# Optimization experiments

Measured on AMD Instinct MI355X. Metric: run time of the kernel, lower is better.

The kernel has to match this reference:

```python
import jax, jax.numpy as jnp
import numpy as np

NDIM = (256, 256, 256)
NMIN = (-1.0, -1.0, -1.0)
NMAX = (1.0, 1.0, 1.0)
NDELTA = tuple((NMAX[i] - NMIN[i]) / (NDIM[i] - 1.0) for i in range(3))
MIN_DEG, MAX_DEG = 0, 10
ANNEALED_ALPHA = 1.0
EPS = 1e-12


def compute_grad(grid):
    # central differences on the voxel grid with edge padding -> [N, 3]
    g = grid.reshape(NDIM[0], NDIM[1], NDIM[2])
    p = jnp.pad(g, ((1, 1), (1, 1), (1, 1)), mode='edge')
    dx = (p[2:, 1:-1, 1:-1] - p[:-2, 1:-1, 1:-1]) / (2.0 * NDELTA[0])
    dy = (p[1:-1, 2:, 1:-1] - p[1:-1, :-2, 1:-1]) / (2.0 * NDELTA[1])
    dz = (p[1:-1, 1:-1, 2:] - p[1:-1, 1:-1, :-2]) / (2.0 * NDELTA[2])
    return jnp.stack([dx, dy, dz], axis=-1).reshape(-1, 3)


def trilinear3(data, pts):
    # data: [N, 4] flattened voxel features, pts: [B, 3] -> [B, 4]
    x = (pts[..., 0] - NMIN[0]) / NDELTA[0]
    y = (pts[..., 1] - NMIN[1]) / NDELTA[1]
    z = (pts[..., 2] - NMIN[2]) / NDELTA[2]
    x0f = jnp.floor(x); y0f = jnp.floor(y); z0f = jnp.floor(z)
    xd = (x - x0f)[..., None]
    yd = (y - y0f)[..., None]
    zd = (z - z0f)[..., None]
    x0 = jnp.clip(x0f.astype(jnp.int32), 0, NDIM[0] - 1)
    x1 = jnp.clip(x0f.astype(jnp.int32) + 1, 0, NDIM[0] - 1)
    y0 = jnp.clip(y0f.astype(jnp.int32), 0, NDIM[1] - 1)
    y1 = jnp.clip(y0f.astype(jnp.int32) + 1, 0, NDIM[1] - 1)
    z0 = jnp.clip(z0f.astype(jnp.int32), 0, NDIM[2] - 1)
    z1 = jnp.clip(z0f.astype(jnp.int32) + 1, 0, NDIM[2] - 1)
    sYZ, sZ = NDIM[1] * NDIM[2], NDIM[2]
    gat = lambda i, j, k: data[sYZ * i + sZ * j + k]
    c00 = gat(x0, y0, z0) * (1 - xd) + gat(x1, y0, z0) * xd
    c01 = gat(x0, y0, z1) * (1 - xd) + gat(x1, y0, z1) * xd
    c10 = gat(x0, y1, z0) * (1 - xd) + gat(x1, y1, z0) * xd
    c11 = gat(x0, y1, z1) * (1 - xd) + gat(x1, y1, z1) * xd
    c0 = c00 * (1 - yd) + c10 * yd
    c1 = c01 * (1 - yd) + c11 * yd
    return c0 * (1 - zd) + c1 * zd


def annealed_pos_enc(x, alpha):
    # nerfies-style windowed positional encoding with identity concat
    bands = jnp.arange(MIN_DEG, MAX_DEG, dtype=x.dtype)  # [D]
    scales = 2.0 ** bands
    xb = x[..., None, :] * scales[:, None]               # [..., D, 3]
    four = jnp.sin(jnp.stack([xb, xb + 0.5 * jnp.pi], axis=-2))  # [..., D, 2, 3]
    w = jnp.clip(alpha - bands, 0.0, 1.0)
    w = 0.5 * (1.0 - jnp.cos(jnp.pi * w))                # cosine easing window
    four = four * w[:, None, None]
    four = four.reshape(x.shape[:-1] + (-1,))            # [..., D*6]
    return jnp.concatenate([x, four], axis=-1)           # [..., 3 + D*6]


def mlp(feats, w0, b0, w1, b1, w2, b2, w3, b3, wo, bo):
    # net_depth=4, skip_layer=2 -> concat inputs after layer index 2
    h = jax.nn.relu(feats @ w0 + b0)
    h = jax.nn.relu(h @ w1 + b1)
    h = jax.nn.relu(h @ w2 + b2)
    h = jnp.concatenate([h, feats], axis=-1)
    h = jax.nn.relu(h @ w3 + b3)
    return h @ wo + bo


def safe_l2_norm(v):
    return jnp.sqrt(jnp.sum(v * v, axis=-1, keepdims=True) + EPS)


def setup_inputs() -> dict:
    key = jax.random.key(0)
    ks = jax.random.split(key, 8)
    B = 1048576
    N = NDIM[0] * NDIM[1] * NDIM[2]
    x = jax.random.uniform(ks[0], (B, 3), jnp.float32, -1.0, 1.0)
    grid = jax.random.normal(ks[1], (N, 1), jnp.float32)
    glorot = lambda k, fi, fo: jax.random.normal(k, (fi, fo), jnp.float32) * jnp.sqrt(2.0 / (fi + fo))
    return {
        'x': x, 'grid': grid,
        'w0': glorot(ks[2], 63, 128), 'b0': jnp.zeros((128,), jnp.float32),
        'w1': glorot(ks[3], 128, 128), 'b1': jnp.zeros((128,), jnp.float32),
        'w2': glorot(ks[4], 128, 128), 'b2': jnp.zeros((128,), jnp.float32),
        'w3': glorot(ks[5], 191, 128), 'b3': jnp.zeros((128,), jnp.float32),
        'wo': jax.random.normal(ks[6], (128, 3), jnp.float32) * 1e-5,  # output_init normal(1e-5)
        'bo': jnp.zeros((3,), jnp.float32),
    }


def reference(x, grid, w0, b0, w1, b1, w2, b2, w3, b3, wo, bo):
    data = jnp.concatenate([grid, compute_grad(grid)], axis=-1)  # [N, 4]
    ret = trilinear3(data, x)                                    # [B, 4]
    feats = annealed_pos_enc(x[:, None], ANNEALED_ALPHA * MAX_DEG)  # [B, 1, 63]
    raw = mlp(feats, w0, b0, w1, b1, w2, b2, w3, b3, wo, bo)[:, 0]  # [B, 3]
    # residual + direct output: rotate gradient vector by axis-angle raw
    theta = safe_l2_norm(raw)
    e = raw / theta
    cond = ret[..., 1:]
    a = safe_l2_norm(cond)
    v = cond / a
    rot = a * (jnp.cos(theta) * v + jnp.sin(theta) * jnp.cross(e, v)
               + (1.0 - jnp.cos(theta)) * jnp.sum(e * v, axis=-1, keepdims=True) * e)
    return (ret[..., :1], ret[..., 1:], rot)
```

## Files before the change

kernel.cpp:

```cpp
#include <hip/hip_runtime.h>


typedef __attribute__((ext_vector_type(4))) float f4;
typedef long long llg;
typedef __attribute__((ext_vector_type(2))) long long llg2;

#define MFMA8 __builtin_amdgcn_mfma_f32_16x16x32_fp8_fp8
#define SCHED_FENCE() __builtin_amdgcn_sched_barrier(0)

__device__ __forceinline__ float bf2f(unsigned int u) {
    union { float f; unsigned int i; } v; v.i = u << 16; return v.f;
}
__device__ __forceinline__ unsigned int pkbf(float a, float b) {
    unsigned int r;
    asm("v_cvt_pk_bf16_f32 %0, %1, %2" : "=v"(r) : "v"(a), "v"(b));
    return r;
}
__device__ __forceinline__ float vfract(float a) {
    float d; asm("v_fract_f32 %0, %1" : "=v"(d) : "v"(a)); return d;
}
__device__ __forceinline__ float vsin(float a) {
    float d; asm("v_sin_f32 %0, %1" : "=v"(d) : "v"(a)); return d;
}
__device__ __forceinline__ float gv(const float* __restrict__ g, int i, int j, int k) {
    return g[(i * 256 + j) * 256 + k];
}
__device__ __forceinline__ int featmap(int kp) {
    if (kp < 3) return kp;
    if (kp == 3) return -1;
    const int m = kp - 4, b = m / 6, r = m - 6 * b, d = r >> 1, c = r & 1;
    return 3 + 6 * b + 3 * c + d;
}
__device__ __forceinline__ int hidperm(int k) {
    const int kt = k >> 5, q = (k >> 3) & 3, j = k & 7;
    return 32 * kt + ((j >> 2) << 4) + (q << 2) + (j & 3);
}
__device__ __forceinline__ llg mkllg(unsigned int lo, unsigned int hi) {
    return (llg)(((unsigned long long)lo) | (((unsigned long long)hi) << 32));
}
__device__ __forceinline__ unsigned int pack8(f4 acc) {
    int d = __builtin_amdgcn_cvt_pk_fp8_f32(fmaxf(acc[0], 0.f), fmaxf(acc[1], 0.f), 0, false);
    d     = __builtin_amdgcn_cvt_pk_fp8_f32(fmaxf(acc[2], 0.f), fmaxf(acc[3], 0.f), d, true);
    return (unsigned int)d;
}

#define WS_TOTAL 67584
#define SWZ_BLOCKS 264
#define DG_BLOCKS 8192
#define DG_OFF_SH 131072
#define WS_NEED (262144ull + 16777216ull * 8ull)
#define WO_SCALE 8192.0f
#define WO_INV   (1.0f / 8192.0f)
#define INV2PI 0.15915494309189535f

__global__ __launch_bounds__(256) void prep(
    const float* __restrict__ g,
    const float* __restrict__ w0, const float* __restrict__ w1,
    const float* __restrict__ w2, const float* __restrict__ w3,
    const float* __restrict__ wo,
    unsigned char* __restrict__ ws8, unsigned short* __restrict__ dg,
    int do_dgrid)
{
    const int bid = blockIdx.x;
    if (bid < SWZ_BLOCKS) {
        int idx = bid * 256 + threadIdx.x;
        const float* src; int base, KTP, Kact, Nact, ld;
        if (idx < 8192)       { src = w0; base = 0;     KTP = 1; Kact = 64;  Nact = 128; ld = 128; }
        else if (idx < 24576) { src = w1; base = 8192;  KTP = 2; Kact = 128; Nact = 128; ld = 128; }
        else if (idx < 40960) { src = w2; base = 24576; KTP = 2; Kact = 128; Nact = 128; ld = 128; }
        else if (idx < 65536) { src = w3; base = 40960; KTP = 3; Kact = 192; Nact = 128; ld = 128; }
        else                  { src = wo; base = 65536; KTP = 2; Kact = 128; Nact = 3;   ld = 3;   }
        int local = idx - base;
        int j    = local & 7;
        int half = (local >> 3) & 1;
        int lane = (local >> 4) & 63;
        int c    = local >> 10;
        int ktp  = c % KTP, nt = c / KTP;
        int kt   = ktp * 2 + half;
        int k = kt * 32 + ((lane >> 4) << 3) + j;
        int n = nt * 16 + (lane & 15);
        float v = 0.0f;
        if (k < Kact && n < Nact) {
            int ko;
            if (base == 0) {
                ko = featmap(k);
            } else if (base == 40960) {
                if (k >= 128) {
                    int f = featmap(k - 128);
                    ko = (f < 0) ? -1 : 128 + f;
                } else {
                    ko = hidperm(k);
                }
            } else {
                ko = hidperm(k);
            }
            if (ko >= 0) v = src[ko * ld + n];
            if (base == 65536) v *= WO_SCALE;
        }
        int p = __builtin_amdgcn_cvt_pk_fp8_f32(v, v, 0, false);
        ws8[idx] = (unsigned char)(p & 0xff);
    } else if (do_dgrid) {
        const int t  = (bid - SWZ_BLOCKS) * 256 + threadIdx.x;
        const int k0 = (t & 31) << 3;
        const int j  = (t >> 5) & 255;
        const int i  = t >> 13;
        const float* row = g + (i * 256 + j) * 256;
        const float* rxp = g + (min(i + 1, 255) * 256 + j) * 256;
        const float* rxm = g + (max(i - 1, 0)   * 256 + j) * 256;
        const float* ryp = g + (i * 256 + min(j + 1, 255)) * 256;
        const float* rym = g + (i * 256 + max(j - 1, 0))   * 256;
        float se[8], sxp[8], sxm[8], syp[8], sym[8];
        {
            f4 a = *(const f4*)(row + k0), b = *(const f4*)(row + k0 + 4);
            #pragma unroll
            for (int q = 0; q < 4; ++q) { se[q] = a[q]; se[q + 4] = b[q]; }
            a = *(const f4*)(rxp + k0); b = *(const f4*)(rxp + k0 + 4);
            #pragma unroll
            for (int q = 0; q < 4; ++q) { sxp[q] = a[q]; sxp[q + 4] = b[q]; }
            a = *(const f4*)(rxm + k0); b = *(const f4*)(rxm + k0 + 4);
            #pragma unroll
            for (int q = 0; q < 4; ++q) { sxm[q] = a[q]; sxm[q + 4] = b[q]; }
            a = *(const f4*)(ryp + k0); b = *(const f4*)(ryp + k0 + 4);
            #pragma unroll
            for (int q = 0; q < 4; ++q) { syp[q] = a[q]; syp[q + 4] = b[q]; }
            a = *(const f4*)(rym + k0); b = *(const f4*)(rym + k0 + 4);
            #pragma unroll
            for (int q = 0; q < 4; ++q) { sym[q] = a[q]; sym[q + 4] = b[q]; }
        }
        float zv[10];
        zv[0] = row[max(k0 - 1, 0)];
        #pragma unroll
        for (int q = 0; q < 8; ++q) zv[q + 1] = se[q];
        zv[9] = row[min(k0 + 8, 255)];
        unsigned int o[16];
        #pragma unroll
        for (int q = 0; q < 8; ++q) {
            o[q * 2 + 0] = pkbf(se[q], (sxp[q] - sxm[q]) * 63.75f);
            o[q * 2 + 1] = pkbf((syp[q] - sym[q]) * 63.75f, (zv[q + 2] - zv[q]) * 63.75f);
        }
        unsigned short* dst = dg + (size_t)(((i * 256 + j) * 256 + k0)) * 4;
        #pragma unroll
        for (int q = 0; q < 4; ++q)
            *(uint4*)(dst + q * 8) = *(const uint4*)(&o[q * 4]);
    }
}

#define FSTRIDE_B 88
#define WV_BYTES (32 * FSTRIDE_B)

#define HIDDEN_LAYER(WSL, BIASP, SRCP, DSTP)                                    \
    do {                                                                        \
        _Pragma("unroll")                                                       \
        for (int utp = 0; utp < 4; ++utp) {                                     \
            const int utA = 2 * utp, utB = 2 * utp + 1;                         \
            llg2 wa0 = *(const llg2*)((WSL) + ((utA * 2 + 0) * 64 + lane) * 16);\
            llg2 wa1 = *(const llg2*)((WSL) + ((utA * 2 + 1) * 64 + lane) * 16);\
            llg2 wb0 = *(const llg2*)((WSL) + ((utB * 2 + 0) * 64 + lane) * 16);\
            llg2 wb1 = *(const llg2*)((WSL) + ((utB * 2 + 1) * 64 + lane) * 16);\
            const f4 biasA = *(const f4*)((BIASP) + utA * 16 + quad * 4);       \
            const f4 biasB = *(const f4*)((BIASP) + utB * 16 + quad * 4);       \
            _Pragma("unroll")                                                   \
            for (int pt = 0; pt < 2; ++pt) {                                    \
                f4 a0 = biasA, a1 = biasB;                                      \
                a0 = MFMA8(wa0[0], SRCP[pt][0], a0, 0, 0, 0);                   \
                a0 = MFMA8(wa0[1], SRCP[pt][1], a0, 0, 0, 0);                   \
                a0 = MFMA8(wa1[0], SRCP[pt][2], a0, 0, 0, 0);                   \
                a0 = MFMA8(wa1[1], SRCP[pt][3], a0, 0, 0, 0);                   \
                a1 = MFMA8(wb0[0], SRCP[pt][0], a1, 0, 0, 0);                   \
                a1 = MFMA8(wb0[1], SRCP[pt][1], a1, 0, 0, 0);                   \
                a1 = MFMA8(wb1[0], SRCP[pt][2], a1, 0, 0, 0);                   \
                a1 = MFMA8(wb1[1], SRCP[pt][3], a1, 0, 0, 0);                   \
                DSTP[pt][utp] = mkllg(pack8(a0), pack8(a1));                    \
            }                                                                   \
            SCHED_FENCE();                                                      \
        }                                                                       \
    } while (0)

template<bool FAST>
__global__ __launch_bounds__(256, 5) void voxmlp(
    const float* __restrict__ x, const float* __restrict__ grid,
    const unsigned char* __restrict__ ws8, const unsigned short* __restrict__ dg,
    const float* __restrict__ b0, const float* __restrict__ b1,
    const float* __restrict__ b2, const float* __restrict__ b3,
    const float* __restrict__ bo,
    float* __restrict__ out, int B)
{
    __shared__ unsigned char smem[WV_BYTES * 4];

    const int lane = threadIdx.x & 63;
    const int wave = threadIdx.x >> 6;
    const int quad = lane >> 4;
    const int lm   = lane & 15;
    unsigned char* fbuf = smem + wave * WV_BYTES;

    const int pbase = blockIdx.x * 128 + wave * 32;

    const int p2   = lane & 31;
    const int role = lane >> 5;
    const int pid  = pbase + p2;

    const float px = x[pid * 3 + 0];
    const float py = x[pid * 3 + 1];
    const float pz = x[pid * 3 + 2];

    if (role == 0) {
        const float fx = (px + 1.0f) * 127.5f;
        const float fy = (py + 1.0f) * 127.5f;
        const float fz = (pz + 1.0f) * 127.5f;
        const float fx0 = floorf(fx), fy0 = floorf(fy), fz0 = floorf(fz);
        const float xd = fx - fx0, yd = fy - fy0, zd = fz - fz0;
        const int ix0 = min(max((int)fx0, 0), 255);
        const int iy0 = min(max((int)fy0, 0), 255);
        const int iz0 = min(max((int)fz0, 0), 255);
        const int ix1 = min(ix0 + 1, 255);
        const int iy1 = min(iy0 + 1, 255);
        const int iz1 = min(iz0 + 1, 255);

        float ret0 = 0.f, c1 = 0.f, c2 = 0.f, c3 = 0.f;
        if (FAST) {
            const unsigned char* dgb = (const unsigned char*)dg;
            const unsigned int vbase = (unsigned int)((ix0 * 65536 + iy0 * 256 + iz0) << 3);
            const unsigned int ox = (unsigned int)((ix1 - ix0) << 19);
            const unsigned int oy = (unsigned int)((iy1 - iy0) << 11);
            const unsigned int oz = (unsigned int)((iz1 - iz0) << 3);
            #pragma unroll
            for (int c = 0; c < 8; ++c) {
                const float wgt = ((c & 4) ? xd : 1.0f - xd) *
                                  ((c & 2) ? yd : 1.0f - yd) *
                                  ((c & 1) ? zd : 1.0f - zd);
                const unsigned int off = vbase + ((c & 4) ? ox : 0u)
                                               + ((c & 2) ? oy : 0u)
                                               + ((c & 1) ? oz : 0u);
                const uint2 w = *(const uint2*)(dgb + off);
                ret0 = fmaf(wgt, bf2f(w.x & 0xffffu), ret0);
                c1   = fmaf(wgt, bf2f(w.x >> 16),     c1);
                c2   = fmaf(wgt, bf2f(w.y & 0xffffu), c2);
                c3   = fmaf(wgt, bf2f(w.y >> 16),     c3);
            }
        } else {
            #pragma unroll
            for (int c = 0; c < 8; ++c) {
                const int i = (c & 4) ? ix1 : ix0;
                const int j = (c & 2) ? iy1 : iy0;
                const int k = (c & 1) ? iz1 : iz0;
                const float wgt = ((c & 4) ? xd : 1.0f - xd) *
                                  ((c & 2) ? yd : 1.0f - yd) *
                                  ((c & 1) ? zd : 1.0f - zd);
                const float v  = gv(grid, i, j, k);
                const float gx = (gv(grid, min(i + 1, 255), j, k) - gv(grid, max(i - 1, 0), j, k)) * 63.75f;
                const float gy = (gv(grid, i, min(j + 1, 255), k) - gv(grid, i, max(j - 1, 0), k)) * 63.75f;
                const float gz = (gv(grid, i, j, min(k + 1, 255)) - gv(grid, i, j, max(k - 1, 0))) * 63.75f;
                ret0 = fmaf(wgt, v,  ret0);
                c1   = fmaf(wgt, gx, c1);
                c2   = fmaf(wgt, gy, c2);
                c3   = fmaf(wgt, gz, c3);
            }
        }
        out[pid] = ret0;
        out[B + pid * 3 + 0] = c1;
        out[B + pid * 3 + 1] = c2;
        out[B + pid * 3 + 2] = c3;
        float* cst = (float*)(fbuf + p2 * FSTRIDE_B + 64);
        cst[0] = c1; cst[1] = c2; cst[2] = c3;
    } else {
        const float r0 = px * INV2PI, r1 = py * INV2PI, r2 = pz * INV2PI;
        unsigned char* fb = fbuf + p2 * FSTRIDE_B;
        auto slotv = [&](int n) -> float {
            if (n == 0) return px;
            if (n == 1) return py;
            if (n == 2) return pz;
            if (n == 3) return 0.0f;
            const int m = n - 4, b = m / 6, t = m % 6, ax = t >> 1, ph = t & 1;
            const float rr = (ax == 0) ? r0 : (ax == 1) ? r1 : r2;
            const float arg = rr * (float)(1 << b) + (ph ? 0.25f : 0.0f);
            return vsin(vfract(arg));
        };
        #pragma unroll
        for (int w = 0; w < 8; ++w) {
            int lo = __builtin_amdgcn_cvt_pk_fp8_f32(slotv(8 * w + 0), slotv(8 * w + 1), 0, false);
            lo     = __builtin_amdgcn_cvt_pk_fp8_f32(slotv(8 * w + 2), slotv(8 * w + 3), lo, true);
            int hi = __builtin_amdgcn_cvt_pk_fp8_f32(slotv(8 * w + 4), slotv(8 * w + 5), 0, false);
            hi     = __builtin_amdgcn_cvt_pk_fp8_f32(slotv(8 * w + 6), slotv(8 * w + 7), hi, true);
            uint2 pk; pk.x = (unsigned int)lo; pk.y = (unsigned int)hi;
            *(uint2*)(fb + w * 8) = pk;
        }
    }
    __builtin_amdgcn_s_barrier();

    const int frow0 = lm * FSTRIDE_B + quad * 8;

    llg actA[2][4];
    llg actB[2][4];
    llg ffp[2][2];

    #pragma unroll
    for (int pt = 0; pt < 2; ++pt)
        #pragma unroll
        for (int kt = 0; kt < 2; ++kt)
            ffp[pt][kt] = *(const llg*)(fbuf + pt * 16 * FSTRIDE_B + frow0 + kt * 32);

    #pragma unroll
    for (int utp = 0; utp < 4; ++utp) {
        const int utA = 2 * utp, utB = 2 * utp + 1;
        llg2 wA = *(const llg2*)(ws8 + (utA * 64 + lane) * 16);
        llg2 wB = *(const llg2*)(ws8 + (utB * 64 + lane) * 16);
        const f4 biasA = *(const f4*)(b0 + utA * 16 + quad * 4);
        const f4 biasB = *(const f4*)(b0 + utB * 16 + quad * 4);
        #pragma unroll
        for (int pt = 0; pt < 2; ++pt) {
            f4 a0 = biasA, a1 = biasB;
            a0 = MFMA8(wA[0], ffp[pt][0], a0, 0, 0, 0);
            a0 = MFMA8(wA[1], ffp[pt][1], a0, 0, 0, 0);
            a1 = MFMA8(wB[0], ffp[pt][0], a1, 0, 0, 0);
            a1 = MFMA8(wB[1], ffp[pt][1], a1, 0, 0, 0);
            actA[pt][utp] = mkllg(pack8(a0), pack8(a1));
        }
        SCHED_FENCE();
    }

    HIDDEN_LAYER(ws8 + 8192,  b1, actA, actB);
    HIDDEN_LAYER(ws8 + 24576, b2, actB, actA);

    #pragma unroll
    for (int utp = 0; utp < 4; ++utp) {
        const int utA = 2 * utp, utB = 2 * utp + 1;
        llg2 ha0 = *(const llg2*)(ws8 + 40960 + ((utA * 3 + 0) * 64 + lane) * 16);
        llg2 ha1 = *(const llg2*)(ws8 + 40960 + ((utA * 3 + 1) * 64 + lane) * 16);
        llg2 ha2 = *(const llg2*)(ws8 + 40960 + ((utA * 3 + 2) * 64 + lane) * 16);
        llg2 hb0 = *(const llg2*)(ws8 + 40960 + ((utB * 3 + 0) * 64 + lane) * 16);
        llg2 hb1 = *(const llg2*)(ws8 + 40960 + ((utB * 3 + 1) * 64 + lane) * 16);
        llg2 hb2 = *(const llg2*)(ws8 + 40960 + ((utB * 3 + 2) * 64 + lane) * 16);
        const f4 biasA = *(const f4*)(b3 + utA * 16 + quad * 4);
        const f4 biasB = *(const f4*)(b3 + utB * 16 + quad * 4);
        #pragma unroll
        for (int pt = 0; pt < 2; ++pt) {
            f4 a0 = biasA, a1 = biasB;
            a0 = MFMA8(ha0[0], actA[pt][0], a0, 0, 0, 0);
            a0 = MFMA8(ha0[1], actA[pt][1], a0, 0, 0, 0);
            a0 = MFMA8(ha1[0], actA[pt][2], a0, 0, 0, 0);
            a0 = MFMA8(ha1[1], actA[pt][3], a0, 0, 0, 0);
            a0 = MFMA8(ha2[0], ffp[pt][0],  a0, 0, 0, 0);
            a0 = MFMA8(ha2[1], ffp[pt][1],  a0, 0, 0, 0);
            a1 = MFMA8(hb0[0], actA[pt][0], a1, 0, 0, 0);
            a1 = MFMA8(hb0[1], actA[pt][1], a1, 0, 0, 0);
            a1 = MFMA8(hb1[0], actA[pt][2], a1, 0, 0, 0);
            a1 = MFMA8(hb1[1], actA[pt][3], a1, 0, 0, 0);
            a1 = MFMA8(hb2[0], ffp[pt][0],  a1, 0, 0, 0);
            a1 = MFMA8(hb2[1], ffp[pt][1],  a1, 0, 0, 0);
            actB[pt][utp] = mkllg(pack8(a0), pack8(a1));
        }
        SCHED_FENCE();
    }

    const llg2 o0 = *(const llg2*)(ws8 + 65536 + (lane * 16));
    const llg2 o1 = *(const llg2*)(ws8 + 65536 + ((64 + lane) * 16));

    const float bo0 = bo[0], bo1 = bo[1], bo2 = bo[2];
    #pragma unroll
    for (int pt = 0; pt < 2; ++pt) {
        f4 acc = {0.f, 0.f, 0.f, 0.f};
        acc = MFMA8(o0[0], actB[pt][0], acc, 0, 0, 0);
        acc = MFMA8(o0[1], actB[pt][1], acc, 0, 0, 0);
        acc = MFMA8(o1[0], actB[pt][2], acc, 0, 0, 0);
        acc = MFMA8(o1[1], actB[pt][3], acc, 0, 0, 0);

        const int pp = pt * 16 + lm;
        const float* cst = (const float*)(fbuf + pp * FSTRIDE_B + 64);
        const float g1 = cst[0], g2 = cst[1], g3 = cst[2];
        const float r0 = acc[0] * WO_INV + bo0;
        const float r1 = acc[1] * WO_INV + bo1;
        const float r2 = acc[2] * WO_INV + bo2;
        const float theta = sqrtf(fmaf(r0, r0, fmaf(r1, r1, r2 * r2)) + 1e-12f);
        const float it = __builtin_amdgcn_rcpf(theta);
        const float e0 = r0 * it, e1 = r1 * it, e2 = r2 * it;
        const float a = sqrtf(fmaf(g1, g1, fmaf(g2, g2, g3 * g3)) + 1e-12f);
        const float ia = __builtin_amdgcn_rcpf(a);
        const float v0 = g1 * ia, v1 = g2 * ia, v2 = g3 * ia;
        const float rv = theta * INV2PI;
        const float st = vsin(vfract(rv));
        const float ct = vsin(vfract(rv + 0.25f));
        const float cx = e1 * v2 - e2 * v1;
        const float cy = e2 * v0 - e0 * v2;
        const float cz = e0 * v1 - e1 * v0;
        const float om = (1.0f - ct) * (e0 * v0 + e1 * v1 + e2 * v2);
        if (quad == 0) {
            const int pid2 = pbase + pp;
            out[4 * B + pid2 * 3 + 0] = a * (ct * v0 + st * cx + om * e0);
            out[4 * B + pid2 * 3 + 1] = a * (ct * v1 + st * cy + om * e1);
            out[4 * B + pid2 * 3 + 2] = a * (ct * v2 + st * cz + om * e2);
        }
    }
}

extern "C" void kernel_launch(void* const* d_in, const int* in_sizes, int n_in,
                              void* d_out, int out_size, void* d_ws, size_t ws_size,
                              hipStream_t stream)
{
    const float* x    = (const float*)d_in[0];
    const float* grid = (const float*)d_in[1];
    const float* w0   = (const float*)d_in[2];
    const float* b0   = (const float*)d_in[3];
    const float* w1   = (const float*)d_in[4];
    const float* b1   = (const float*)d_in[5];
    const float* w2   = (const float*)d_in[6];
    const float* b2   = (const float*)d_in[7];
    const float* w3   = (const float*)d_in[8];
    const float* b3   = (const float*)d_in[9];
    const float* wo   = (const float*)d_in[10];
    const float* bo   = (const float*)d_in[11];
    float* out = (float*)d_out;
    unsigned char* ws8 = (unsigned char*)d_ws;
    unsigned short* dg = (unsigned short*)d_ws + DG_OFF_SH;

    const int B = in_sizes[0] / 3;
    const int fast = (ws_size >= WS_NEED) ? 1 : 0;
    const int nprep = fast ? (SWZ_BLOCKS + DG_BLOCKS) : SWZ_BLOCKS;
    prep<<<nprep, 256, 0, stream>>>(grid, w0, w1, w2, w3, wo, ws8, dg, fast);
    if (fast)
        voxmlp<true><<<B / 128, 256, 0, stream>>>(x, grid, ws8, dg, b0, b1, b2, b3, bo, out, B);
    else
        voxmlp<false><<<B / 128, 256, 0, stream>>>(x, grid, ws8, dg, b0, b1, b2, b3, bo, out, B);
}
```

Measured before the change: 322.1 us.

## Process two 32-point batches per wave to amortize weight loads and gathers

Each wave now handles 64 points (two 32-point sub-batches) instead of 32, so the grid shrinks by half. Trilinear gathers for both batches are issued together (role 0 lanes) and positional encoding for both is computed by role 1 lanes. The MLP body then runs twice back to back, reusing the same weight loads from cache. LDS per block doubles, and running the MLP twice serially may raise register pressure and reduce occupancy; B must now be divisible by 256.

```diff
diff --git a/kernel.cpp b/kernel.cpp
--- a/kernel.cpp
+++ b/kernel.cpp
@@ -4,6 +4,7 @@
 typedef __attribute__((ext_vector_type(4))) float f4;
 typedef long long llg;
 typedef __attribute__((ext_vector_type(2))) long long llg2;
+typedef unsigned long long u64;
 
 #define MFMA8 __builtin_amdgcn_mfma_f32_16x16x32_fp8_fp8
 #define SCHED_FENCE() __builtin_amdgcn_sched_barrier(0)
@@ -147,6 +148,68 @@
 
 #define FSTRIDE_B 88
 #define WV_BYTES (32 * FSTRIDE_B)
+#define WV2 (2 * WV_BYTES)
+
+#define TRI_SETUP(S, PX, PY, PZ)                                               \
+    const float fx##S = ((PX) + 1.0f) * 127.5f;                                \
+    const float fy##S = ((PY) + 1.0f) * 127.5f;                                \
+    const float fz##S = ((PZ) + 1.0f) * 127.5f;                                \
+    const float fx0##S = floorf(fx##S), fy0##S = floorf(fy##S), fz0##S = floorf(fz##S); \
+    const float xd##S = fx##S - fx0##S, yd##S = fy##S - fy0##S, zd##S = fz##S - fz0##S; \
+    const int ix0##S = min(max((int)fx0##S, 0), 255);                          \
+    const int iy0##S = min(max((int)fy0##S, 0), 255);                          \
+    const int iz0##S = min(max((int)fz0##S, 0), 255);                          \
+    const int ix1##S = min(ix0##S + 1, 255);                                   \
+    const int iy1##S = min(iy0##S + 1, 255);                                   \
+    const int iz1##S = min(iz0##S + 1, 255);
+
+#define POSENC(PX, PY, PZ, FB)                                                 \
+    do {                                                                       \
+        const float r0_ = (PX) * INV2PI, r1_ = (PY) * INV2PI, r2_ = (PZ) * INV2PI; \
+        unsigned char* fb_ = (FB);                                             \
+        auto slotv_ = [&](int n) -> float {                                    \
+            if (n == 0) return (PX);                                           \
+            if (n == 1) return (PY);                                           \
+            if (n == 2) return (PZ);                                           \
+            if (n == 3) return 0.0f;                                           \
+            const int m_ = n - 4, b_ = m_ / 6, t_ = m_ % 6, ax_ = t_ >> 1, ph_ = t_ & 1; \
+            const float rr_ = (ax_ == 0) ? r0_ : (ax_ == 1) ? r1_ : r2_;       \
+            const float arg_ = rr_ * (float)(1 << b_) + (ph_ ? 0.25f : 0.0f);  \
+            return vsin(vfract(arg_));                                         \
+        };                                                                     \
+        _Pragma("unroll")                                                      \
+        for (int w_ = 0; w_ < 8; ++w_) {                                       \
+            int lo_ = __builtin_amdgcn_cvt_pk_fp8_f32(slotv_(8 * w_ + 0), slotv_(8 * w_ + 1), 0, false); \
+            lo_     = __builtin_amdgcn_cvt_pk_fp8_f32(slotv_(8 * w_ + 2), slotv_(8 * w_ + 3), lo_, true); \
+            int hi_ = __builtin_amdgcn_cvt_pk_fp8_f32(slotv_(8 * w_ + 4), slotv_(8 * w_ + 5), 0, false); \
+            hi_     = __builtin_amdgcn_cvt_pk_fp8_f32(slotv_(8 * w_ + 6), slotv_(8 * w_ + 7), hi_, true); \
+            uint2 pk_; pk_.x = (unsigned int)lo_; pk_.y = (unsigned int)hi_;   \
+            *(uint2*)(fb_ + w_ * 8) = pk_;                                     \
+        }                                                                      \
+    } while (0)
+
+#define CONSUME(S, GL, PIDX, FB)                                               \
+    do {                                                                       \
+        float ret0_ = 0.f, c1_ = 0.f, c2_ = 0.f, c3_ = 0.f;                    \
+        _Pragma("unroll")                                                      \
+        for (int c_ = 0; c_ < 8; ++c_) {                                       \
+            const float wgt_ = ((c_ & 4) ? xd##S : 1.0f - xd##S) *             \
+                               ((c_ & 2) ? yd##S : 1.0f - yd##S) *             \
+                               ((c_ & 1) ? zd##S : 1.0f - zd##S);              \
+            const unsigned int wx_ = (unsigned int)(GL)[c_];                   \
+            const unsigned int wy_ = (unsigned int)((GL)[c_] >> 32);           \
+            ret0_ = fmaf(wgt_, bf2f(wx_ & 0xffffu), ret0_);                    \
+            c1_   = fmaf(wgt_, bf2f(wx_ >> 16),     c1_);                      \
+            c2_   = fmaf(wgt_, bf2f(wy_ & 0xffffu), c2_);                      \
+            c3_   = fmaf(wgt_, bf2f(wy_ >> 16),     c3_);                      \
+        }                                                                      \
+        out[(PIDX)] = ret0_;                                                   \
+        out[B + (PIDX) * 3 + 0] = c1_;                                         \
+        out[B + (PIDX) * 3 + 1] = c2_;                                         \
+        out[B + (PIDX) * 3 + 2] = c3_;                                         \
+        float* cst_ = (float*)((FB) + p2 * FSTRIDE_B + 64);                    \
+        cst_[0] = c1_; cst_[1] = c2_; cst_[2] = c3_;                           \
+    } while (0)
 
 #define HIDDEN_LAYER(WSL, BIASP, SRCP, DSTP)                                    \
     do {                                                                        \
@@ -176,6 +239,105 @@
         }                                                                       \
     } while (0)
 
+#define MLP_BODY(FBUF, PB)                                                      \
+    do {                                                                        \
+        const int frow0 = lm * FSTRIDE_B + quad * 8;                            \
+        llg actA[2][4];                                                         \
+        llg actB[2][4];                                                         \
+        llg ffp[2][2];                                                          \
+        _Pragma("unroll")                                                       \
+        for (int pt = 0; pt < 2; ++pt)                                          \
+            _Pragma("unroll")                                                   \
+            for (int kt = 0; kt < 2; ++kt)                                      \
+                ffp[pt][kt] = *(const llg*)((FBUF) + pt * 16 * FSTRIDE_B + frow0 + kt * 32); \
+        _Pragma("unroll")                                                       \
+        for (int utp = 0; utp < 4; ++utp) {                                     \
+            const int utA = 2 * utp, utB = 2 * utp + 1;                         \
+            llg2 wA = *(const llg2*)(ws8 + (utA * 64 + lane) * 16);             \
+            llg2 wB = *(const llg2*)(ws8 + (utB * 64 + lane) * 16);             \
+            const f4 biasA = *(const f4*)(b0 + utA * 16 + quad * 4);            \
+            const f4 biasB = *(const f4*)(b0 + utB * 16 + quad * 4);            \
+            _Pragma("unroll")                                                   \
+            for (int pt = 0; pt < 2; ++pt) {                                    \
+                f4 a0 = biasA, a1 = biasB;                                      \
+                a0 = MFMA8(wA[0], ffp[pt][0], a0, 0, 0, 0);                     \
+                a0 = MFMA8(wA[1], ffp[pt][1], a0, 0, 0, 0);                     \
+                a1 = MFMA8(wB[0], ffp[pt][0], a1, 0, 0, 0);                     \
+                a1 = MFMA8(wB[1], ffp[pt][1], a1, 0, 0, 0);                     \
+                actA[pt][utp] = mkllg(pack8(a0), pack8(a1));                    \
+            }                                                                   \
+            SCHED_FENCE();                                                      \
+        }                                                                       \
+        HIDDEN_LAYER(ws8 + 8192,  b1, actA, actB);                              \
+        HIDDEN_LAYER(ws8 + 24576, b2, actB, actA);                              \
+        _Pragma("unroll")                                                       \
+        for (int utp = 0; utp < 4; ++utp) {                                     \
+            const int utA = 2 * utp, utB = 2 * utp + 1;                         \
+            llg2 ha0 = *(const llg2*)(ws8 + 40960 + ((utA * 3 + 0) * 64 + lane) * 16); \
+            llg2 ha1 = *(const llg2*)(ws8 + 40960 + ((utA * 3 + 1) * 64 + lane) * 16); \
+            llg2 ha2 = *(const llg2*)(ws8 + 40960 + ((utA * 3 + 2) * 64 + lane) * 16); \
+            llg2 hb0 = *(const llg2*)(ws8 + 40960 + ((utB * 3 + 0) * 64 + lane) * 16); \
+            llg2 hb1 = *(const llg2*)(ws8 + 40960 + ((utB * 3 + 1) * 64 + lane) * 16); \
+            llg2 hb2 = *(const llg2*)(ws8 + 40960 + ((utB * 3 + 2) * 64 + lane) * 16); \
+            const f4 biasA = *(const f4*)(b3 + utA * 16 + quad * 4);            \
+            const f4 biasB = *(const f4*)(b3 + utB * 16 + quad * 4);            \
+            _Pragma("unroll")                                                   \
+            for (int pt = 0; pt < 2; ++pt) {                                    \
+                f4 a0 = biasA, a1 = biasB;                                      \
+                a0 = MFMA8(ha0[0], actA[pt][0], a0, 0, 0, 0);                   \
+                a0 = MFMA8(ha0[1], actA[pt][1], a0, 0, 0, 0);                   \
+                a0 = MFMA8(ha1[0], actA[pt][2], a0, 0, 0, 0);                   \
+                a0 = MFMA8(ha1[1], actA[pt][3], a0, 0, 0, 0);                   \
+                a0 = MFMA8(ha2[0], ffp[pt][0],  a0, 0, 0, 0);                   \
+                a0 = MFMA8(ha2[1], ffp[pt][1],  a0, 0, 0, 0);                   \
+                a1 = MFMA8(hb0[0], actA[pt][0], a1, 0, 0, 0);                   \
+                a1 = MFMA8(hb0[1], actA[pt][1], a1, 0, 0, 0);                   \
+                a1 = MFMA8(hb1[0], actA[pt][2], a1, 0, 0, 0);                   \
+                a1 = MFMA8(hb1[1], actA[pt][3], a1, 0, 0, 0);                   \
+                a1 = MFMA8(hb2[0], ffp[pt][0],  a1, 0, 0, 0);                   \
+                a1 = MFMA8(hb2[1], ffp[pt][1],  a1, 0, 0, 0);                   \
+                actB[pt][utp] = mkllg(pack8(a0), pack8(a1));                    \
+            }                                                                   \
+            SCHED_FENCE();                                                      \
+        }                                                                       \
+        const llg2 o0 = *(const llg2*)(ws8 + 65536 + (lane * 16));              \
+        const llg2 o1 = *(const llg2*)(ws8 + 65536 + ((64 + lane) * 16));       \
+        const float bo0 = bo[0], bo1 = bo[1], bo2 = bo[2];                      \
+        _Pragma("unroll")                                                       \
+        for (int pt = 0; pt < 2; ++pt) {                                        \
+            f4 acc = {0.f, 0.f, 0.f, 0.f};                                      \
+            acc = MFMA8(o0[0], actB[pt][0], acc, 0, 0, 0);                      \
+            acc = MFMA8(o0[1], actB[pt][1], acc, 0, 0, 0);                      \
+            acc = MFMA8(o1[0], actB[pt][2], acc, 0, 0, 0);                      \
+            acc = MFMA8(o1[1], actB[pt][3], acc, 0, 0, 0);                      \
+            const int pp = pt * 16 + lm;                                        \
+            const float* cst = (const float*)((FBUF) + pp * FSTRIDE_B + 64);    \
+            const float g1 = cst[0], g2 = cst[1], g3 = cst[2];                  \
+            const float r0 = acc[0] * WO_INV + bo0;                             \
+            const float r1 = acc[1] * WO_INV + bo1;                             \
+            const float r2 = acc[2] * WO_INV + bo2;                             \
+            const float theta = sqrtf(fmaf(r0, r0, fmaf(r1, r1, r2 * r2)) + 1e-12f); \
+            const float it = __builtin_amdgcn_rcpf(theta);                      \
+            const float e0 = r0 * it, e1 = r1 * it, e2 = r2 * it;               \
+            const float a = sqrtf(fmaf(g1, g1, fmaf(g2, g2, g3 * g3)) + 1e-12f); \
+            const float ia = __builtin_amdgcn_rcpf(a);                          \
+            const float v0 = g1 * ia, v1 = g2 * ia, v2 = g3 * ia;               \
+            const float rv = theta * INV2PI;                                    \
+            const float st = vsin(vfract(rv));                                  \
+            const float ct = vsin(vfract(rv + 0.25f));                          \
+            const float cx = e1 * v2 - e2 * v1;                                 \
+            const float cy = e2 * v0 - e0 * v2;                                 \
+            const float cz = e0 * v1 - e1 * v0;                                 \
+            const float om = (1.0f - ct) * (e0 * v0 + e1 * v1 + e2 * v2);       \
+            if (quad == 0) {                                                    \
+                const int pid2 = (PB) + pp;                                     \
+                out[4 * B + pid2 * 3 + 0] = a * (ct * v0 + st * cx + om * e0);  \
+                out[4 * B + pid2 * 3 + 1] = a * (ct * v1 + st * cy + om * e1);  \
+                out[4 * B + pid2 * 3 + 2] = a * (ct * v2 + st * cz + om * e2);  \
+            }                                                                   \
+        }                                                                       \
+    } while (0)
+
 template<bool FAST>
 __global__ __launch_bounds__(256, 5) void voxmlp(
     const float* __restrict__ x, const float* __restrict__ grid,
@@ -185,211 +347,135 @@
     const float* __restrict__ bo,
     float* __restrict__ out, int B)
 {
-    __shared__ unsigned char smem[WV_BYTES * 4];
+    __shared__ unsigned char smem[WV2 * 4];
 
     const int lane = threadIdx.x & 63;
     const int wave = threadIdx.x >> 6;
     const int quad = lane >> 4;
     const int lm   = lane & 15;
-    unsigned char* fbuf = smem + wave * WV_BYTES;
-
-    const int pbase = blockIdx.x * 128 + wave * 32;
+    unsigned char* fbufA = smem + wave * WV2;
+    unsigned char* fbufB = fbufA + WV_BYTES;
+
+    const int pbase = blockIdx.x * 256 + wave * 64;
 
     const int p2   = lane & 31;
     const int role = lane >> 5;
-    const int pid  = pbase + p2;
-
-    const float px = x[pid * 3 + 0];
-    const float py = x[pid * 3 + 1];
-    const float pz = x[pid * 3 + 2];
-
-    if (role == 0) {
-        const float fx = (px + 1.0f) * 127.5f;
-        const float fy = (py + 1.0f) * 127.5f;
-        const float fz = (pz + 1.0f) * 127.5f;
-        const float fx0 = floorf(fx), fy0 = floorf(fy), fz0 = floorf(fz);
-        const float xd = fx - fx0, yd = fy - fy0, zd = fz - fz0;
-        const int ix0 = min(max((int)fx0, 0), 255);
-        const int iy0 = min(max((int)fy0, 0), 255);
-        const int iz0 = min(max((int)fz0, 0), 255);
-        const int ix1 = min(ix0 + 1, 255);
-        const int iy1 = min(iy0 + 1, 255);
-        const int iz1 = min(iz0 + 1, 255);
-
-        float ret0 = 0.f, c1 = 0.f, c2 = 0.f, c3 = 0.f;
-        if (FAST) {
-            const unsigned char* dgb = (const unsigned char*)dg;
-            const unsigned int vbase = (unsigned int)((ix0 * 65536 + iy0 * 256 + iz0) << 3);
-            const unsigned int ox = (unsigned int)((ix1 - ix0) << 19);
-            const unsigned int oy = (unsigned int)((iy1 - iy0) << 11);
-            const unsigned int oz = (unsigned int)((iz1 - iz0) << 3);
-            #pragma unroll
-            for (int c = 0; c < 8; ++c) {
-                const float wgt = ((c & 4) ? xd : 1.0f - xd) *
-                                  ((c & 2) ? yd : 1.0f - yd) *
-                                  ((c & 1) ? zd : 1.0f - zd);
-                const unsigned int off = vbase + ((c & 4) ? ox : 0u)
-                                               + ((c & 2) ? oy : 0u)
-                                               + ((c & 1) ? oz : 0u);
-                const uint2 w = *(const uint2*)(dgb + off);
-                ret0 = fmaf(wgt, bf2f(w.x & 0xffffu), ret0);
-                c1   = fmaf(wgt, bf2f(w.x >> 16),     c1);
-                c2   = fmaf(wgt, bf2f(w.y & 0xffffu), c2);
-                c3   = fmaf(wgt, bf2f(w.y >> 16),     c3);
+    const int pidA = pbase + p2;
+    const int pidB = pbase + 32 + p2;
+
+    const float pxA = x[pidA * 3 + 0];
+    const float pyA = x[pidA * 3 + 1];
+    const float pzA = x[pidA * 3 + 2];
+    const float pxB = x[pidB * 3 + 0];
+    const float pyB = x[pidB * 3 + 1];
+    const float pzB = x[pidB * 3 + 2];
+
+    if (FAST) {
+        const unsigned char* dgb = (const unsigned char*)dg;
+        TRI_SETUP(A, pxA, pyA, pzA)
+        TRI_SETUP(B, pxB, pyB, pzB)
+        const unsigned int vbA = (unsigned int)((ix0A * 65536 + iy0A * 256 + iz0A) << 3);
+        const unsigned int oxA = (unsigned int)((ix1A - ix0A) << 19);
+        const unsigned int oyA = (unsigned int)((iy1A - iy0A) << 11);
+        const unsigned int ozA = (unsigned int)((iz1A - iz0A) << 3);
+        const unsigned int vbB = (unsigned int)((ix0B * 65536 + iy0B * 256 + iz0B) << 3);
+        const unsigned int oxB = (unsigned int)((ix1B - ix0B) << 19);
+        const unsigned int oyB = (unsigned int)((iy1B - iy0B) << 11);
+        const unsigned int ozB = (unsigned int)((iz1B - iz0B) << 3);
+
+        u64 glA[8], glB[8];
+        #pragma unroll
+        for (int c = 0; c < 8; ++c) {
+            const unsigned int off = vbA + ((c & 4) ? oxA : 0u)
+                                         + ((c & 2) ? oyA : 0u)
+                                         + ((c & 1) ? ozA : 0u);
+            glA[c] = *(const u64*)(dgb + off);
+        }
+        #pragma unroll
+        for (int c = 0; c < 8; ++c) {
+            const unsigned int off = vbB + ((c & 4) ? oxB : 0u)
+                                         + ((c & 2) ? oyB : 0u)
+                                         + ((c & 1) ? ozB : 0u);
+            glB[c] = *(const u64*)(dgb + off);
+        }
+        #pragma unroll
+        for (int c = 0; c < 8; ++c) {
+            asm volatile("" : "+v"(glA[c]));
+            asm volatile("" : "+v"(glB[c]));
+        }
+
+        if (role == 1) {
+            POSENC(pxA, pyA, pzA, fbufA + p2 * FSTRIDE_B);
+            POSENC(pxB, pyB, pzB, fbufB + p2 * FSTRIDE_B);
+        } else {
+            CONSUME(A, glA, pidA, fbufA);
+            CONSUME(B, glB, pidB, fbufB);
+        }
+    } else {
+        if (role == 0) {
+            TRI_SETUP(A, pxA, pyA, pzA)
+            {
+                float ret0 = 0.f, c1 = 0.f, c2 = 0.f, c3 = 0.f;
+                #pragma unroll
+                for (int c = 0; c < 8; ++c) {
+                    const int i = (c & 4) ? ix1A : ix0A;
+                    const int j = (c & 2) ? iy1A : iy0A;
+                    const int k = (c & 1) ? iz1A : iz0A;
+                    const float wgt = ((c & 4) ? xdA : 1.0f - xdA) *
+                                      ((c & 2) ? ydA : 1.0f - ydA) *
+                                      ((c & 1) ? zdA : 1.0f - zdA);
+                    const float v  = gv(grid, i, j, k);
+                    const float gx = (gv(grid, min(i + 1, 255), j, k) - gv(grid, max(i - 1, 0), j, k)) * 63.75f;
+                    const float gy = (gv(grid, i, min(j + 1, 255), k) - gv(grid, i, max(j - 1, 0), k)) * 63.75f;
+                    const float gz = (gv(grid, i, j, min(k + 1, 255)) - gv(grid, i, j, max(k - 1, 0))) * 63.75f;
+                    ret0 = fmaf(wgt, v,  ret0);
+                    c1   = fmaf(wgt, gx, c1);
+                    c2   = fmaf(wgt, gy, c2);
+                    c3   = fmaf(wgt, gz, c3);
+                }
+                out[pidA] = ret0;
+                out[B + pidA * 3 + 0] = c1;
+                out[B + pidA * 3 + 1] = c2;
+                out[B + pidA * 3 + 2] = c3;
+                float* cst = (float*)(fbufA + p2 * FSTRIDE_B + 64);
+                cst[0] = c1; cst[1] = c2; cst[2] = c3;
+            }
+            TRI_SETUP(B, pxB, pyB, pzB)
+            {
+                float ret0 = 0.f, c1 = 0.f, c2 = 0.f, c3 = 0.f;
+                #pragma unroll
+                for (int c = 0; c < 8; ++c) {
+                    const int i = (c & 4) ? ix1B : ix0B;
+                    const int j = (c & 2) ? iy1B : iy0B;
+                    const int k = (c & 1) ? iz1B : iz0B;
+                    const float wgt = ((c & 4) ? xdB : 1.0f - xdB) *
+                                      ((c & 2) ? ydB : 1.0f - ydB) *
+                                      ((c & 1) ? zdB : 1.0f - zdB);
+                    const float v  = gv(grid, i, j, k);
+                    const float gx = (gv(grid, min(i + 1, 255), j, k) - gv(grid, max(i - 1, 0), j, k)) * 63.75f;
+                    const float gy = (gv(grid, i, min(j + 1, 255), k) - gv(grid, i, max(j - 1, 0), k)) * 63.75f;
+                    const float gz = (gv(grid, i, j, min(k + 1, 255)) - gv(grid, i, j, max(k - 1, 0))) * 63.75f;
+                    ret0 = fmaf(wgt, v,  ret0);
+                    c1   = fmaf(wgt, gx, c1);
+                    c2   = fmaf(wgt, gy, c2);
+                    c3   = fmaf(wgt, gz, c3);
+                }
+                out[pidB] = ret0;
+                out[B + pidB * 3 + 0] = c1;
+                out[B + pidB * 3 + 1] = c2;
+                out[B + pidB * 3 + 2] = c3;
+                float* cst = (float*)(fbufB + p2 * FSTRIDE_B + 64);
+                cst[0] = c1; cst[1] = c2; cst[2] = c3;
             }
         } else {
-            #pragma unroll
-            for (int c = 0; c < 8; ++c) {
-                const int i = (c & 4) ? ix1 : ix0;
-                const int j = (c & 2) ? iy1 : iy0;
-                const int k = (c & 1) ? iz1 : iz0;
-                const float wgt = ((c & 4) ? xd : 1.0f - xd) *
-                                  ((c & 2) ? yd : 1.0f - yd) *
-                                  ((c & 1) ? zd : 1.0f - zd);
-                const float v  = gv(grid, i, j, k);
-                const float gx = (gv(grid, min(i + 1, 255), j, k) - gv(grid, max(i - 1, 0), j, k)) * 63.75f;
-                const float gy = (gv(grid, i, min(j + 1, 255), k) - gv(grid, i, max(j - 1, 0), k)) * 63.75f;
-                const float gz = (gv(grid, i, j, min(k + 1, 255)) - gv(grid, i, j, max(k - 1, 0))) * 63.75f;
-                ret0 = fmaf(wgt, v,  ret0);
-                c1   = fmaf(wgt, gx, c1);
-                c2   = fmaf(wgt, gy, c2);
-                c3   = fmaf(wgt, gz, c3);
-            }
-        }
-        out[pid] = ret0;
-        out[B + pid * 3 + 0] = c1;
-        out[B + pid * 3 + 1] = c2;
-        out[B + pid * 3 + 2] = c3;
-        float* cst = (float*)(fbuf + p2 * FSTRIDE_B + 64);
-        cst[0] = c1; cst[1] = c2; cst[2] = c3;
-    } else {
-        const float r0 = px * INV2PI, r1 = py * INV2PI, r2 = pz * INV2PI;
-        unsigned char* fb = fbuf + p2 * FSTRIDE_B;
-        auto slotv = [&](int n) -> float {
-            if (n == 0) return px;
-            if (n == 1) return py;
-            if (n == 2) return pz;
-            if (n == 3) return 0.0f;
-            const int m = n - 4, b = m / 6, t = m % 6, ax = t >> 1, ph = t & 1;
-            const float rr = (ax == 0) ? r0 : (ax == 1) ? r1 : r2;
-            const float arg = rr * (float)(1 << b) + (ph ? 0.25f : 0.0f);
-            return vsin(vfract(arg));
-        };
-        #pragma unroll
-        for (int w = 0; w < 8; ++w) {
-            int lo = __builtin_amdgcn_cvt_pk_fp8_f32(slotv(8 * w + 0), slotv(8 * w + 1), 0, false);
-            lo     = __builtin_amdgcn_cvt_pk_fp8_f32(slotv(8 * w + 2), slotv(8 * w + 3), lo, true);
-            int hi = __builtin_amdgcn_cvt_pk_fp8_f32(slotv(8 * w + 4), slotv(8 * w + 5), 0, false);
-            hi     = __builtin_amdgcn_cvt_pk_fp8_f32(slotv(8 * w + 6), slotv(8 * w + 7), hi, true);
-            uint2 pk; pk.x = (unsigned int)lo; pk.y = (unsigned int)hi;
-            *(uint2*)(fb + w * 8) = pk;
+            POSENC(pxA, pyA, pzA, fbufA + p2 * FSTRIDE_B);
+            POSENC(pxB, pyB, pzB, fbufB + p2 * FSTRIDE_B);
         }
     }
     __builtin_amdgcn_s_barrier();
 
-    const int frow0 = lm * FSTRIDE_B + quad * 8;
-
-    llg actA[2][4];
-    llg actB[2][4];
-    llg ffp[2][2];
-
-    #pragma unroll
-    for (int pt = 0; pt < 2; ++pt)
-        #pragma unroll
-        for (int kt = 0; kt < 2; ++kt)
-            ffp[pt][kt] = *(const llg*)(fbuf + pt * 16 * FSTRIDE_B + frow0 + kt * 32);
-
-    #pragma unroll
-    for (int utp = 0; utp < 4; ++utp) {
-        const int utA = 2 * utp, utB = 2 * utp + 1;
-        llg2 wA = *(const llg2*)(ws8 + (utA * 64 + lane) * 16);
-        llg2 wB = *(const llg2*)(ws8 + (utB * 64 + lane) * 16);
-        const f4 biasA = *(const f4*)(b0 + utA * 16 + quad * 4);
-        const f4 biasB = *(const f4*)(b0 + utB * 16 + quad * 4);
-        #pragma unroll
-        for (int pt = 0; pt < 2; ++pt) {
-            f4 a0 = biasA, a1 = biasB;
-            a0 = MFMA8(wA[0], ffp[pt][0], a0, 0, 0, 0);
-            a0 = MFMA8(wA[1], ffp[pt][1], a0, 0, 0, 0);
-            a1 = MFMA8(wB[0], ffp[pt][0], a1, 0, 0, 0);
-            a1 = MFMA8(wB[1], ffp[pt][1], a1, 0, 0, 0);
-            actA[pt][utp] = mkllg(pack8(a0), pack8(a1));
-        }
-        SCHED_FENCE();
-    }
-
-    HIDDEN_LAYER(ws8 + 8192,  b1, actA, actB);
-    HIDDEN_LAYER(ws8 + 24576, b2, actB, actA);
-
-    #pragma unroll
-    for (int utp = 0; utp < 4; ++utp) {
-        const int utA = 2 * utp, utB = 2 * utp + 1;
-        llg2 ha0 = *(const llg2*)(ws8 + 40960 + ((utA * 3 + 0) * 64 + lane) * 16);
-        llg2 ha1 = *(const llg2*)(ws8 + 40960 + ((utA * 3 + 1) * 64 + lane) * 16);
-        llg2 ha2 = *(const llg2*)(ws8 + 40960 + ((utA * 3 + 2) * 64 + lane) * 16);
-        llg2 hb0 = *(const llg2*)(ws8 + 40960 + ((utB * 3 + 0) * 64 + lane) * 16);
-        llg2 hb1 = *(const llg2*)(ws8 + 40960 + ((utB * 3 + 1) * 64 + lane) * 16);
-        llg2 hb2 = *(const llg2*)(ws8 + 40960 + ((utB * 3 + 2) * 64 + lane) * 16);
-        const f4 biasA = *(const f4*)(b3 + utA * 16 + quad * 4);
-        const f4 biasB = *(const f4*)(b3 + utB * 16 + quad * 4);
-        #pragma unroll
-        for (int pt = 0; pt < 2; ++pt) {
-            f4 a0 = biasA, a1 = biasB;
-            a0 = MFMA8(ha0[0], actA[pt][0], a0, 0, 0, 0);
-            a0 = MFMA8(ha0[1], actA[pt][1], a0, 0, 0, 0);
-            a0 = MFMA8(ha1[0], actA[pt][2], a0, 0, 0, 0);
-            a0 = MFMA8(ha1[1], actA[pt][3], a0, 0, 0, 0);
-            a0 = MFMA8(ha2[0], ffp[pt][0],  a0, 0, 0, 0);
-            a0 = MFMA8(ha2[1], ffp[pt][1],  a0, 0, 0, 0);
-            a1 = MFMA8(hb0[0], actA[pt][0], a1, 0, 0, 0);
-            a1 = MFMA8(hb0[1], actA[pt][1], a1, 0, 0, 0);
-            a1 = MFMA8(hb1[0], actA[pt][2], a1, 0, 0, 0);
-            a1 = MFMA8(hb1[1], actA[pt][3], a1, 0, 0, 0);
-            a1 = MFMA8(hb2[0], ffp[pt][0],  a1, 0, 0, 0);
-            a1 = MFMA8(hb2[1], ffp[pt][1],  a1, 0, 0, 0);
-            actB[pt][utp] = mkllg(pack8(a0), pack8(a1));
-        }
-        SCHED_FENCE();
-    }
-
-    const llg2 o0 = *(const llg2*)(ws8 + 65536 + (lane * 16));
-    const llg2 o1 = *(const llg2*)(ws8 + 65536 + ((64 + lane) * 16));
-
-    const float bo0 = bo[0], bo1 = bo[1], bo2 = bo[2];
-    #pragma unroll
-    for (int pt = 0; pt < 2; ++pt) {
-        f4 acc = {0.f, 0.f, 0.f, 0.f};
-        acc = MFMA8(o0[0], actB[pt][0], acc, 0, 0, 0);
-        acc = MFMA8(o0[1], actB[pt][1], acc, 0, 0, 0);
-        acc = MFMA8(o1[0], actB[pt][2], acc, 0, 0, 0);
-        acc = MFMA8(o1[1], actB[pt][3], acc, 0, 0, 0);
-
-        const int pp = pt * 16 + lm;
-        const float* cst = (const float*)(fbuf + pp * FSTRIDE_B + 64);
-        const float g1 = cst[0], g2 = cst[1], g3 = cst[2];
-        const float r0 = acc[0] * WO_INV + bo0;
-        const float r1 = acc[1] * WO_INV + bo1;
-        const float r2 = acc[2] * WO_INV + bo2;
-        const float theta = sqrtf(fmaf(r0, r0, fmaf(r1, r1, r2 * r2)) + 1e-12f);
-        const float it = __builtin_amdgcn_rcpf(theta);
-        const float e0 = r0 * it, e1 = r1 * it, e2 = r2 * it;
-        const float a = sqrtf(fmaf(g1, g1, fmaf(g2, g2, g3 * g3)) + 1e-12f);
-        const float ia = __builtin_amdgcn_rcpf(a);
-        const float v0 = g1 * ia, v1 = g2 * ia, v2 = g3 * ia;
-        const float rv = theta * INV2PI;
-        const float st = vsin(vfract(rv));
-        const float ct = vsin(vfract(rv + 0.25f));
-        const float cx = e1 * v2 - e2 * v1;
-        const float cy = e2 * v0 - e0 * v2;
-        const float cz = e0 * v1 - e1 * v0;
-        const float om = (1.0f - ct) * (e0 * v0 + e1 * v1 + e2 * v2);
-        if (quad == 0) {
-            const int pid2 = pbase + pp;
-            out[4 * B + pid2 * 3 + 0] = a * (ct * v0 + st * cx + om * e0);
-            out[4 * B + pid2 * 3 + 1] = a * (ct * v1 + st * cy + om * e1);
-            out[4 * B + pid2 * 3 + 2] = a * (ct * v2 + st * cz + om * e2);
-        }
-    }
+    MLP_BODY(fbufA, pbase);
+    MLP_BODY(fbufB, pbase + 32);
 }
 
 extern "C" void kernel_launch(void* const* d_in, const int* in_sizes, int n_in,
@@ -417,7 +503,7 @@
     const int nprep = fast ? (SWZ_BLOCKS + DG_BLOCKS) : SWZ_BLOCKS;
     prep<<<nprep, 256, 0, stream>>>(grid, w0, w1, w2, w3, wo, ws8, dg, fast);
     if (fast)
-        voxmlp<true><<<B / 128, 256, 0, stream>>>(x, grid, ws8, dg, b0, b1, b2, b3, bo, out, B);
+        voxmlp<true><<<B / 256, 256, 0, stream>>>(x, grid, ws8, dg, b0, b1, b2, b3, bo, out, B);
     else
-        voxmlp<false><<<B / 128, 256, 0, stream>>>(x, grid, ws8, dg, b0, b1, b2, b3, bo, out, B);
-}
+        voxmlp<false><<<B / 256, 256, 0, stream>>>(x, grid, ws8, dg, b0, b1, b2, b3, bo, out, B);
+}
```

Measured after the change: 451.9 us. 40.3% more time.
